# Kernel optimization log

Measured on AMD Instinct MI355X. Metric: run time of the kernel, lower is better.

The kernel has to match this reference:

```python
import jax, jax.numpy as jnp
import numpy as np

N = 50000
E = 500000
IN_DIM = 384
HID = 64
HEADS = 4
OUT_DIM = 128
EPS_SM = 1e-16
EPS_LN = 1e-5
NEG_SLOPE = 0.2


def gat_conv(x, row, col, ew, W, a_src, a_dst, b, heads, out_ch, concat):
    n = x.shape[0]
    h = (x @ W).reshape(n, heads, out_ch)              # [N, H, C]
    # per-node attention scores, then gather (same math as gathering h first)
    s_src = jnp.sum(h * a_src, axis=-1)                # [N, H]
    s_dst = jnp.sum(h * a_dst, axis=-1)                # [N, H]
    alpha = jax.nn.leaky_relu(s_src[row] + s_dst[col], NEG_SLOPE)  # [E, H]
    alpha = alpha * ew[:, None]
    a_exp = jnp.exp(alpha)
    denom = jax.ops.segment_sum(a_exp, col, num_segments=n)        # [N, H]
    alpha = a_exp / (denom[col] + EPS_SM)              # [E, H]
    msg = alpha[:, :, None] * h[col]                   # [E, H, C]
    out = jax.ops.segment_sum(msg, row, num_segments=n)  # [N, H, C]
    if concat:
        out = out.reshape(n, heads * out_ch)
    else:
        out = out.mean(axis=1)
    return out + b


def layer_norm(x, g, b):
    mu = x.mean(axis=-1, keepdims=True)
    var = x.var(axis=-1, keepdims=True)
    return (x - mu) / jnp.sqrt(var + EPS_LN) * g + b


def setup_inputs() -> dict:
    key = jax.random.key(0)
    ks = jax.random.split(key, 16)
    D1 = HEADS * HID  # 256
    inp = {
        "x": jax.random.normal(ks[0], (N, IN_DIM), jnp.float32),
        "edge_index": jax.random.randint(ks[1], (2, E), 0, N, jnp.int32),
        "edge_weight": jax.random.uniform(ks[2], (E,), jnp.float32),
        "W1": jax.random.normal(ks[3], (IN_DIM, D1), jnp.float32) * (1.0 / np.sqrt(IN_DIM)),
        "as1": jax.random.normal(ks[4], (1, HEADS, HID), jnp.float32) * 0.1,
        "ad1": jax.random.normal(ks[5], (1, HEADS, HID), jnp.float32) * 0.1,
        "b1": jnp.zeros((D1,), jnp.float32),
        "g1": jnp.ones((D1,), jnp.float32),
        "be1": jnp.zeros((D1,), jnp.float32),
        "W2": jax.random.normal(ks[6], (D1, D1), jnp.float32) * (1.0 / np.sqrt(D1)),
        "as2": jax.random.normal(ks[7], (1, HEADS, HID), jnp.float32) * 0.1,
        "ad2": jax.random.normal(ks[8], (1, HEADS, HID), jnp.float32) * 0.1,
        "b2": jnp.zeros((D1,), jnp.float32),
        "g2": jnp.ones((D1,), jnp.float32),
        "be2": jnp.zeros((D1,), jnp.float32),
        "W3": jax.random.normal(ks[9], (D1, OUT_DIM), jnp.float32) * (1.0 / np.sqrt(D1)),
        "as3": jax.random.normal(ks[10], (1, 1, OUT_DIM), jnp.float32) * 0.1,
        "ad3": jax.random.normal(ks[11], (1, 1, OUT_DIM), jnp.float32) * 0.1,
        "b3": jnp.zeros((OUT_DIM,), jnp.float32),
        "g3": jnp.ones((OUT_DIM,), jnp.float32),
        "be3": jnp.zeros((OUT_DIM,), jnp.float32),
    }
    return inp


def reference(x, edge_index, edge_weight, W1, as1, ad1, b1, g1, be1,
              W2, as2, ad2, b2, g2, be2, W3, as3, ad3, b3, g3, be3):
    row, col = edge_index[0], edge_index[1]
    h = gat_conv(x, row, col, edge_weight, W1, as1, ad1, b1, HEADS, HID, True)
    h = jax.nn.elu(layer_norm(h, g1, be1))
    h = gat_conv(h, row, col, edge_weight, W2, as2, ad2, b2, HEADS, HID, True)
    h = jax.nn.elu(layer_norm(h, g2, be2))
    h = gat_conv(h, row, col, edge_weight, W3, as3, ad3, b3, 1, OUT_DIM, False)
    return layer_norm(h, g3, be3)
```

## Files before the change

### kernel.cpp

```cpp
#include <hip/hip_runtime.h>
#include <hip/hip_bf16.h>


typedef __bf16 bf16x8_t __attribute__((ext_vector_type(8)));
typedef float  fx4      __attribute__((ext_vector_type(4)));

__device__ __forceinline__ float u2f(unsigned short u) {
    return __uint_as_float(((unsigned)u) << 16);
}
__device__ __forceinline__ unsigned short f2u(float f) {
    unsigned b = __float_as_uint(f);
    unsigned rounded = b + 0x7FFF + ((b >> 16) & 1);
    if (((b >> 23) & 0xFF) == 0xFF) rounded = b;
    return (unsigned short)(rounded >> 16);
}

__global__ void f32_to_bf16_k(const float* __restrict__ src, unsigned short* __restrict__ dst,
                              long n) {
    long i = (long)blockIdx.x * 256 + threadIdx.x;
    const long stride = (long)gridDim.x * 256;
    for (; i < n; i += stride) dst[i] = f2u(src[i]);
}

__global__ void transpose_conv_k(const float* __restrict__ W, unsigned short* __restrict__ Wt,
                                 int K, int N) {
    int idx = blockIdx.x * 256 + threadIdx.x;
    if (idx >= K * N) return;
    int k = idx / N, n = idx - k * N;
    Wt[(size_t)n * K + k] = f2u(W[idx]);
}

__global__ void fill_const_f32_k(float* __restrict__ out, long n, float v) {
    long i = (long)blockIdx.x * 256 + threadIdx.x;
    const long stride = (long)gridDim.x * 256;
    for (; i < n; i += stride) out[i] = v;
}

__global__ void count_both_k(const int* __restrict__ row, const int* __restrict__ col,
                             int* __restrict__ rcnt, int* __restrict__ ccnt,
                             int2* __restrict__ rank, int E, int Nn) {
    int e = blockIdx.x * 256 + threadIdx.x;
    if (e >= E) return;
    int r = row[e], c = col[e];
    int rr = -1, rc = -1;
    if ((unsigned)r < (unsigned)Nn) rr = atomicAdd(&rcnt[r], 1);
    if ((unsigned)c < (unsigned)Nn) rc = atomicAdd(&ccnt[c], 1);
    rank[e] = make_int2(rr, rc);
}

__global__ __launch_bounds__(256) void scan1_k(const int* __restrict__ cnt,
                                               int* __restrict__ local,
                                               int* __restrict__ bsum, int n) {
    __shared__ int sm[256];
    int i = blockIdx.x * 256 + threadIdx.x;
    int tid = threadIdx.x;
    int v = (i < n) ? cnt[i] : 0;
    sm[tid] = v;
    __syncthreads();
    for (int o = 1; o < 256; o <<= 1) {
        int t = (tid >= o) ? sm[tid - o] : 0;
        __syncthreads();
        sm[tid] += t;
        __syncthreads();
    }
    if (i < n) local[i] = sm[tid];
    if (tid == 255) bsum[blockIdx.x] = sm[255];
}

__global__ __launch_bounds__(512) void scan2_k(int* __restrict__ bsum, int nb) {
    __shared__ int sm[512];
    int tid = threadIdx.x;
    int v = (tid < nb) ? bsum[tid] : 0;
    sm[tid] = v;
    __syncthreads();
    for (int o = 1; o < 512; o <<= 1) {
        int t = (tid >= o) ? sm[tid - o] : 0;
        __syncthreads();
        sm[tid] += t;
        __syncthreads();
    }
    if (tid < nb) bsum[tid] = sm[tid];
}

__global__ __launch_bounds__(256) void scan3_k(const int* __restrict__ cnt,
                                               const int* __restrict__ local,
                                               const int* __restrict__ bsum,
                                               int* __restrict__ rowptr,
                                               int* __restrict__ colptr,
                                               int N) {
    int i = blockIdx.x * 256 + threadIdx.x;
    int n2 = 2 * N;
    if (i >= n2) return;
    int b = blockIdx.x;
    int s = local[i] + (b > 0 ? bsum[b - 1] : 0);
    if (i < N) {
        rowptr[i + 1] = s;
        if (i == 0) rowptr[0] = 0;
    } else {
        int bN = (N - 1) >> 8;
        int base = local[N - 1] + (bN > 0 ? bsum[bN - 1] : 0);
        int j = i - N;
        colptr[j + 1] = s - base;
        if (j == 0) colptr[0] = 0;
    }
}

__global__ void fill_both_k(const int* __restrict__ row, const int* __restrict__ col,
                            const float* __restrict__ ew,
                            const int2* __restrict__ rank,
                            const int* __restrict__ rowptr, const int* __restrict__ colptr,
                            long* __restrict__ csr, long* __restrict__ csc,
                            int E, int Nn) {
    int e = blockIdx.x * 256 + threadIdx.x;
    if (e >= E) return;
    int r = row[e], c = col[e];
    int wb = __float_as_int(ew[e]);
    int2 rk = rank[e];
    if (rk.x >= 0) {
        int s = rowptr[r] + rk.x;
        int cc = ((unsigned)c < (unsigned)Nn) ? c : 0;
        long v = (long)(unsigned)cc | ((long)(unsigned)wb << 32);
        __builtin_nontemporal_store(v, csr + s);
    }
    if (rk.y >= 0) {
        int s = colptr[c] + rk.y;
        int rr = ((unsigned)r < (unsigned)Nn) ? r : 0;
        long v = (long)(unsigned)rr | ((long)(unsigned)wb << 32);
        __builtin_nontemporal_store(v, csc + s);
    }
}

#define LSTR 40
__global__ __launch_bounds__(256) void gemm_bf16(const unsigned short* __restrict__ A,
                                                 const unsigned short* __restrict__ Bt,
                                                 unsigned short* __restrict__ C,
                                                 int M, int Ncol, int K) {
    __shared__ unsigned short As[128 * LSTR];
    __shared__ unsigned short Bs[128 * LSTR];
    const int t = threadIdx.x;
    const int lane = t & 63;
    const int wave = t >> 6;
    const int quad = lane >> 4, l16 = lane & 15;
    const int row0 = blockIdx.y * 128, col0 = blockIdx.x * 128;
    const int wr = (wave >> 1) * 64, wc = (wave & 1) * 64;
    const int sr = t >> 2, ss = (t & 3) * 8;
    fx4 acc[4][4] = {};
    for (int k0 = 0; k0 < K; k0 += 32) {
#pragma unroll
        for (int rr = 0; rr < 2; rr++) {
            int r = sr + rr * 64;
            uint4 av = make_uint4(0, 0, 0, 0);
            int gr = row0 + r;
            if (gr < M) av = *(const uint4*)(A + (size_t)gr * K + k0 + ss);
            *(uint4*)(As + r * LSTR + ss) = av;
            uint4 bv = *(const uint4*)(Bt + (size_t)(col0 + r) * K + k0 + ss);
            *(uint4*)(Bs + r * LSTR + ss) = bv;
        }
        __syncthreads();
        bf16x8_t af[4], bfr[4];
#pragma unroll
        for (int i = 0; i < 4; i++) {
            af[i]  = *(const bf16x8_t*)(As + (wr + i * 16 + l16) * LSTR + quad * 8);
            bfr[i] = *(const bf16x8_t*)(Bs + (wc + i * 16 + l16) * LSTR + quad * 8);
        }
#pragma unroll
        for (int i = 0; i < 4; i++)
#pragma unroll
            for (int j = 0; j < 4; j++)
                acc[i][j] = __builtin_amdgcn_mfma_f32_16x16x32_bf16(af[i], bfr[j], acc[i][j], 0, 0, 0);
        __syncthreads();
    }
#pragma unroll
    for (int i = 0; i < 4; i++) {
        int rb = row0 + wr + i * 16 + quad * 4;
#pragma unroll
        for (int j = 0; j < 4; j++) {
            int c = col0 + wc + j * 16 + l16;
#pragma unroll
            for (int r = 0; r < 4; r++) {
                int gr = rb + r;
                if (gr < M) C[(size_t)gr * Ncol + c] = f2u(acc[i][j][r]);
            }
        }
    }
}

template <int CPL, int LPH, int H>
__global__ __launch_bounds__(256) void scores_k(const unsigned short* __restrict__ hb,
                                                const float* __restrict__ asrc,
                                                const float* __restrict__ adst,
                                                float* __restrict__ ssrc, float* __restrict__ sdst,
                                                int N) {
    int node = blockIdx.x * 4 + (threadIdx.x >> 6);
    if (node >= N) return;
    int lane = threadIdx.x & 63;
    const int D = CPL * 64;
    const unsigned short* hp = hb + (size_t)node * D + lane * CPL;
    float s1 = 0.f, s2 = 0.f;
#pragma unroll
    for (int i = 0; i < CPL; i++) {
        float h = u2f(hp[i]);
        s1 += h * asrc[lane * CPL + i];
        s2 += h * adst[lane * CPL + i];
    }
#pragma unroll
    for (int m = 1; m < LPH; m <<= 1) {
        s1 += __shfl_xor(s1, m);
        s2 += __shfl_xor(s2, m);
    }
    if ((lane & (LPH - 1)) == 0) {
        ssrc[(size_t)node * H + lane / LPH] = s1;
        sdst[(size_t)node * H + lane / LPH] = s2;
    }
}

template <int H>
__global__ __launch_bounds__(256) void denom_csc_k(const int* __restrict__ colptr,
                                                   const int2* __restrict__ csc,
                                                   const float* __restrict__ ssrc,
                                                   const float* __restrict__ sdst,
                                                   float* __restrict__ att, int N) {
    int idx = blockIdx.x * 256 + threadIdx.x;
    int node = idx / H;
    int h = idx - node * H;
    if (node >= N) return;
    const float sd = sdst[(size_t)node * H + h];
    float acc = 0.f;
    int kbeg = colptr[node], kend = colptr[node + 1];
    if (kbeg < kend) {
        int klast = kend - 1;
        int2 ceA = csc[kbeg];
        int2 ceB = csc[(kbeg + 1 < kend) ? kbeg + 1 : klast];
        int2 ceC = csc[(kbeg + 2 < kend) ? kbeg + 2 : klast];
        float sA = ssrc[(size_t)ceA.x * H + h];
        float sB = ssrc[(size_t)ceB.x * H + h];
        for (int k = kbeg; k < kend; k++) {
            int2 ceD = csc[(k + 3 < kend) ? k + 3 : klast];
            float sC = ssrc[(size_t)ceC.x * H + h];
            float we = __int_as_float(ceA.y);
            float s = sA + sd;
            s = (s > 0.f) ? s : 0.2f * s;
            acc += __expf(fminf(s * we, 60.f));
            ceA = ceB; ceB = ceC; ceC = ceD;
            sA = sB; sB = sC;
        }
    }
    att[(size_t)node * 2 * H + h] = sd;
    att[(size_t)node * 2 * H + H + h] = 1.0f / (acc + 1e-16f);
}

template <int CPL, int H, bool DOELU, bool F32OUT>
__global__ __launch_bounds__(256) void agg_ln_k(const unsigned short* __restrict__ hb,
                                                const float* __restrict__ ssrc,
                                                const float* __restrict__ att,
                                                const int* __restrict__ rowptr,
                                                const int2* __restrict__ csr,
                                                const float* __restrict__ bias,
                                                const float* __restrict__ gamma,
                                                const float* __restrict__ beta,
                                                void* __restrict__ outv, int N, int E) {
    int node = blockIdx.x * 4 + (threadIdx.x >> 6);
    if (node >= N) return;
    const int lane = threadIdx.x & 63;
    const int hl = lane & 31;
    const int eo = lane >> 5;
    const int D = CPL * 32, C = D / H;
    const int colbase = hl * CPL;
    const int head = colbase / C;
    const float sn = ssrc[(size_t)node * H + head];
    const unsigned short* hbl = hb + colbase;
    float acc[CPL] = {};
    int kbeg = rowptr[node], kend = rowptr[node + 1];
    if (kbeg < 0) kbeg = 0;
    if (kend > E) kend = E;

    if (kbeg < kend) {
        const int klast = kend - 1;
        int kA = kbeg + eo, kB = kbeg + 2 + eo, kC = kbeg + 4 + eo;
        int2 ceA = csr[kA < kend ? kA : klast];
        int2 ceB = csr[kB < kend ? kB : klast];
        int2 ceC = csr[kC < kend ? kC : klast];
        float sdA, rdA, sdB, rdB;
        uint4 hvA = make_uint4(0,0,0,0), hvB = make_uint4(0,0,0,0);
        {
            const float* ap = att + (size_t)ceA.x * (2 * H);
            if constexpr (H == 1) { float2 p = *(const float2*)ap; sdA = p.x; rdA = p.y; }
            else { sdA = ap[head]; rdA = ap[H + head]; }
            const unsigned short* hp = hbl + (size_t)ceA.x * D;
            if constexpr (CPL == 8) hvA = *(const uint4*)hp;
            else { uint2 t2 = *(const uint2*)hp; hvA.x = t2.x; hvA.y = t2.y; }
        }
        {
            const float* ap = att + (size_t)ceB.x * (2 * H);
            if constexpr (H == 1) { float2 p = *(const float2*)ap; sdB = p.x; rdB = p.y; }
            else { sdB = ap[head]; rdB = ap[H + head]; }
            const unsigned short* hp = hbl + (size_t)ceB.x * D;
            if constexpr (CPL == 8) hvB = *(const uint4*)hp;
            else { uint2 t2 = *(const uint2*)hp; hvB.x = t2.x; hvB.y = t2.y; }
        }
        for (int k = kbeg; k < kend; k += 2) {
            int kD = k + 6 + eo;
            int2 ceD = csr[kD < kend ? kD : klast];
            float sdC, rdC;
            uint4 hvC = make_uint4(0,0,0,0);
            {
                const float* ap = att + (size_t)ceC.x * (2 * H);
                if constexpr (H == 1) { float2 p = *(const float2*)ap; sdC = p.x; rdC = p.y; }
                else { sdC = ap[head]; rdC = ap[H + head]; }
                const unsigned short* hp = hbl + (size_t)ceC.x * D;
                if constexpr (CPL == 8) hvC = *(const uint4*)hp;
                else { uint2 t2 = *(const uint2*)hp; hvC.x = t2.x; hvC.y = t2.y; }
            }
            float we = __int_as_float(ceA.y);
            float s = sn + sdA;
            s = (s > 0.f) ? s : 0.2f * s;
            float ae = __expf(fminf(s * we, 60.f));
            float w = ae * rdA;
            w = (k + eo < kend) ? w : 0.f;
            acc[0] += w * u2f((unsigned short)(hvA.x & 0xFFFFu));
            acc[1] += w * u2f((unsigned short)(hvA.x >> 16));
            acc[2] += w * u2f((unsigned short)(hvA.y & 0xFFFFu));
            acc[3] += w * u2f((unsigned short)(hvA.y >> 16));
            if constexpr (CPL == 8) {
                acc[4] += w * u2f((unsigned short)(hvA.z & 0xFFFFu));
                acc[5] += w * u2f((unsigned short)(hvA.z >> 16));
                acc[6] += w * u2f((unsigned short)(hvA.w & 0xFFFFu));
                acc[7] += w * u2f((unsigned short)(hvA.w >> 16));
            }
            ceA = ceB; ceB = ceC; ceC = ceD;
            sdA = sdB; rdA = rdB; hvA = hvB;
            sdB = sdC; rdB = rdC; hvB = hvC;
        }
    }
#pragma unroll
    for (int i = 0; i < CPL; i++) acc[i] += __shfl_xor(acc[i], 32);

    float v[CPL];
    float sum = 0.f, sq = 0.f;
#pragma unroll
    for (int i = 0; i < CPL; i++) {
        v[i] = acc[i] + bias[colbase + i];
        sum += v[i];
        sq += v[i] * v[i];
    }
#pragma unroll
    for (int m = 1; m < 32; m <<= 1) {
        sum += __shfl_xor(sum, m);
        sq += __shfl_xor(sq, m);
    }
    float mu  = sum * (1.0f / D);
    float var = sq * (1.0f / D) - mu * mu;
    float inv = rsqrtf(fmaxf(var, 0.f) + 1e-5f);
    if (eo == 0) {
#pragma unroll
        for (int i = 0; i < CPL; i++) {
            float y = (v[i] - mu) * inv * gamma[colbase + i] + beta[colbase + i];
            if (DOELU) y = (y > 0.f) ? y : (__expf(y) - 1.f);
            size_t idx = (size_t)node * D + colbase + i;
            if constexpr (F32OUT) ((float*)outv)[idx] = y;
            else                  ((unsigned short*)outv)[idx] = f2u(y);
        }
    }
}

extern "C" void kernel_launch(void* const* d_in, const int* in_sizes, int n_in,
                              void* d_out, int out_size, void* d_ws, size_t ws_size,
                              hipStream_t stream) {
    const int IN_DIM = 384;
    const int N = in_sizes[0] / IN_DIM;
    const int E = in_sizes[1] / 2;
    float* outp = (float*)d_out;
    const int FG = 2048;

    if (n_in != 21 || out_size != N * 128) {
        fill_const_f32_k<<<FG, 256, 0, stream>>>(outp, (long)out_size, 9.0f);
        return;
    }

    const float* x = (const float*)d_in[0];
    const int* ei = (const int*)d_in[1];
    const int* row = ei;
    const int* col = ei + E;
    const float* ew = (const float*)d_in[2];
    const float* W1 = (const float*)d_in[3];
    const float* as1 = (const float*)d_in[4];
    const float* ad1 = (const float*)d_in[5];
    const float* b1 = (const float*)d_in[6];
    const float* g1 = (const float*)d_in[7];
    const float* be1 = (const float*)d_in[8];
    const float* W2 = (const float*)d_in[9];
    const float* as2 = (const float*)d_in[10];
    const float* ad2 = (const float*)d_in[11];
    const float* b2 = (const float*)d_in[12];
    const float* g2 = (const float*)d_in[13];
    const float* be2 = (const float*)d_in[14];
    const float* W3 = (const float*)d_in[15];
    const float* as3 = (const float*)d_in[16];
    const float* ad3 = (const float*)d_in[17];
    const float* b3 = (const float*)d_in[18];
    const float* g3 = (const float*)d_in[19];
    const float* be3 = (const float*)d_in[20];

    char* ws = (char*)d_ws;
    size_t off = 0;
    auto alloc = [&](size_t b) -> char* {
        char* p = ws + off;
        off = (off + b + 255) & ~(size_t)255;
        return p;
    };
    unsigned short* xb = (unsigned short*)alloc((size_t)N * IN_DIM * 2);
    unsigned short* hb = (unsigned short*)alloc((size_t)N * 256 * 2);
    unsigned short* ab = (unsigned short*)alloc((size_t)N * 256 * 2);
    float* att = (float*)alloc((size_t)N * 8 * 4);
    float* ssrc = (float*)alloc((size_t)N * 4 * 4);
    float* sdst = (float*)alloc((size_t)N * 4 * 4);
    unsigned short* W1t = (unsigned short*)alloc((size_t)384 * 256 * 2);
    unsigned short* W2t = (unsigned short*)alloc((size_t)256 * 256 * 2);
    unsigned short* W3t = (unsigned short*)alloc((size_t)256 * 128 * 2);
    int* rowptr = (int*)alloc((size_t)(N + 1) * 4);
    int* colptr = (int*)alloc((size_t)(N + 1) * 4);
    int* cnt2 = (int*)alloc((size_t)2 * N * 4);
    int* slocal = (int*)alloc((size_t)2 * N * 4);
    int* sbsum = (int*)alloc((size_t)512 * 4);
    int2* rank = (int2*)alloc((size_t)E * 8);
    long* csr = (long*)alloc((size_t)E * 8);
    long* csc = (long*)alloc((size_t)E * 8);

    if (off > ws_size) {
        fill_const_f32_k<<<FG, 256, 0, stream>>>(outp, (long)out_size, 7.0f);
        return;
    }

    int* rcnt = cnt2;
    int* ccnt = cnt2 + N;

    const int ebl = (E + 255) / 256;
    const int nbl4 = (N + 3) / 4;
    const int mrows = (N + 127) / 128;
    const int n2 = 2 * N;
    const int sblocks = (n2 + 255) / 256;

    f32_to_bf16_k<<<FG, 256, 0, stream>>>(x, xb, (long)N * IN_DIM);
    transpose_conv_k<<<(384 * 256 + 255) / 256, 256, 0, stream>>>(W1, W1t, 384, 256);
    transpose_conv_k<<<(256 * 256 + 255) / 256, 256, 0, stream>>>(W2, W2t, 256, 256);
    transpose_conv_k<<<(256 * 128 + 255) / 256, 256, 0, stream>>>(W3, W3t, 256, 128);

    hipMemsetAsync(cnt2, 0, (size_t)n2 * 4, stream);
    count_both_k<<<ebl, 256, 0, stream>>>(row, col, rcnt, ccnt, rank, E, N);
    scan1_k<<<sblocks, 256, 0, stream>>>(cnt2, slocal, sbsum, n2);
    scan2_k<<<1, 512, 0, stream>>>(sbsum, sblocks);
    scan3_k<<<sblocks, 256, 0, stream>>>(cnt2, slocal, sbsum, rowptr, colptr, N);
    fill_both_k<<<ebl, 256, 0, stream>>>(row, col, ew, rank, rowptr, colptr, csr, csc, E, N);

    gemm_bf16<<<dim3(2, mrows), 256, 0, stream>>>(xb, W1t, hb, N, 256, 384);
    scores_k<4, 16, 4><<<nbl4, 256, 0, stream>>>(hb, as1, ad1, ssrc, sdst, N);
    denom_csc_k<4><<<(N * 4 + 255) / 256, 256, 0, stream>>>(colptr, (const int2*)csc, ssrc, sdst, att, N);
    agg_ln_k<8, 4, true, false><<<nbl4, 256, 0, stream>>>(hb, ssrc, att, rowptr, (const int2*)csr,
                                                          b1, g1, be1, ab, N, E);

    gemm_bf16<<<dim3(2, mrows), 256, 0, stream>>>(ab, W2t, hb, N, 256, 256);
    scores_k<4, 16, 4><<<nbl4, 256, 0, stream>>>(hb, as2, ad2, ssrc, sdst, N);
    denom_csc_k<4><<<(N * 4 + 255) / 256, 256, 0, stream>>>(colptr, (const int2*)csc, ssrc, sdst, att, N);
    agg_ln_k<8, 4, true, false><<<nbl4, 256, 0, stream>>>(hb, ssrc, att, rowptr, (const int2*)csr,
                                                          b2, g2, be2, ab, N, E);

    gemm_bf16<<<dim3(1, mrows), 256, 0, stream>>>(ab, W3t, hb, N, 128, 256);
    scores_k<2, 64, 1><<<nbl4, 256, 0, stream>>>(hb, as3, ad3, ssrc, sdst, N);
    denom_csc_k<1><<<(N + 255) / 256, 256, 0, stream>>>(colptr, (const int2*)csc, ssrc, sdst, att, N);
    agg_ln_k<4, 1, false, true><<<nbl4, 256, 0, stream>>>(hb, ssrc, att, rowptr, (const int2*)csr,
                                                          b3, g3, be3, outp, N, E);
}
```

Baseline: 505.8 us.

## Split edge loops across more lanes in denominator and aggregation kernels

The softmax-denominator kernel now gives each (node, head) pair two threads that stride over alternate incoming edges, then combines their partial sums with a lane shuffle. The aggregation kernel now has each wavefront handle four edges at a time instead of two. Each lane covers twice as many feature columns through two 16-byte loads, and the partial results are reduced across lane groups. The aim is more memory-level parallelism on the irregular edge gathers of short adjacency lists, at the cost of more registers per lane and extra shuffle reductions.

```diff
diff --git a/kernel.cpp b/kernel.cpp
--- a/kernel.cpp
+++ b/kernel.cpp
@@ -221,21 +221,27 @@
                                                    const float* __restrict__ sdst,
                                                    float* __restrict__ att, int N) {
     int idx = blockIdx.x * 256 + threadIdx.x;
-    int node = idx / H;
-    int h = idx - node * H;
+    const int L2H = (H == 4) ? 2 : ((H == 2) ? 1 : 0);
+    int node = idx >> (L2H + 1);
+    int rem = idx - (node << (L2H + 1));
+    int h = rem & (H - 1);
+    int parity = rem >> L2H;
     if (node >= N) return;
     const float sd = sdst[(size_t)node * H + h];
     float acc = 0.f;
     int kbeg = colptr[node], kend = colptr[node + 1];
-    if (kbeg < kend) {
+    int k0 = kbeg + parity;
+    if (k0 < kend) {
         int klast = kend - 1;
-        int2 ceA = csc[kbeg];
-        int2 ceB = csc[(kbeg + 1 < kend) ? kbeg + 1 : klast];
-        int2 ceC = csc[(kbeg + 2 < kend) ? kbeg + 2 : klast];
+        int kB = k0 + 2, kC = k0 + 4;
+        int2 ceA = csc[k0];
+        int2 ceB = csc[kB < kend ? kB : klast];
+        int2 ceC = csc[kC < kend ? kC : klast];
         float sA = ssrc[(size_t)ceA.x * H + h];
         float sB = ssrc[(size_t)ceB.x * H + h];
-        for (int k = kbeg; k < kend; k++) {
-            int2 ceD = csc[(k + 3 < kend) ? k + 3 : klast];
+        for (int k = k0; k < kend; k += 2) {
+            int kD = k + 6;
+            int2 ceD = csc[kD < kend ? kD : klast];
             float sC = ssrc[(size_t)ceC.x * H + h];
             float we = __int_as_float(ceA.y);
             float s = sA + sd;
@@ -245,8 +251,11 @@
             sA = sB; sB = sC;
         }
     }
-    att[(size_t)node * 2 * H + h] = sd;
-    att[(size_t)node * 2 * H + H + h] = 1.0f / (acc + 1e-16f);
+    acc += __shfl_xor(acc, H);
+    if (parity == 0) {
+        att[(size_t)node * 2 * H + h] = sd;
+        att[(size_t)node * 2 * H + H + h] = 1.0f / (acc + 1e-16f);
+    }
 }
 
 template <int CPL, int H, bool DOELU, bool F32OUT>
@@ -262,10 +271,10 @@
     int node = blockIdx.x * 4 + (threadIdx.x >> 6);
     if (node >= N) return;
     const int lane = threadIdx.x & 63;
-    const int hl = lane & 31;
-    const int eo = lane >> 5;
-    const int D = CPL * 32, C = D / H;
-    const int colbase = hl * CPL;
+    const int ql = lane & 15;
+    const int eo = lane >> 4;
+    const int D = CPL * 16, C = D / H;
+    const int colbase = ql * CPL;
     const int head = colbase / C;
     const float sn = ssrc[(size_t)node * H + head];
     const unsigned short* hbl = hb + colbase;
@@ -276,40 +285,41 @@
 
     if (kbeg < kend) {
         const int klast = kend - 1;
-        int kA = kbeg + eo, kB = kbeg + 2 + eo, kC = kbeg + 4 + eo;
+        int kA = kbeg + eo, kB = kbeg + 4 + eo, kC = kbeg + 8 + eo;
         int2 ceA = csr[kA < kend ? kA : klast];
         int2 ceB = csr[kB < kend ? kB : klast];
         int2 ceC = csr[kC < kend ? kC : klast];
         float sdA, rdA, sdB, rdB;
-        uint4 hvA = make_uint4(0,0,0,0), hvB = make_uint4(0,0,0,0);
+        uint4 hvA0 = make_uint4(0,0,0,0), hvA1 = make_uint4(0,0,0,0);
+        uint4 hvB0 = make_uint4(0,0,0,0), hvB1 = make_uint4(0,0,0,0);
         {
             const float* ap = att + (size_t)ceA.x * (2 * H);
             if constexpr (H == 1) { float2 p = *(const float2*)ap; sdA = p.x; rdA = p.y; }
             else { sdA = ap[head]; rdA = ap[H + head]; }
             const unsigned short* hp = hbl + (size_t)ceA.x * D;
-            if constexpr (CPL == 8) hvA = *(const uint4*)hp;
-            else { uint2 t2 = *(const uint2*)hp; hvA.x = t2.x; hvA.y = t2.y; }
+            hvA0 = *(const uint4*)hp;
+            if constexpr (CPL == 16) hvA1 = *(const uint4*)(hp + 8);
         }
         {
             const float* ap = att + (size_t)ceB.x * (2 * H);
             if constexpr (H == 1) { float2 p = *(const float2*)ap; sdB = p.x; rdB = p.y; }
             else { sdB = ap[head]; rdB = ap[H + head]; }
             const unsigned short* hp = hbl + (size_t)ceB.x * D;
-            if constexpr (CPL == 8) hvB = *(const uint4*)hp;
-            else { uint2 t2 = *(const uint2*)hp; hvB.x = t2.x; hvB.y = t2.y; }
-        }
-        for (int k = kbeg; k < kend; k += 2) {
-            int kD = k + 6 + eo;
+            hvB0 = *(const uint4*)hp;
+            if constexpr (CPL == 16) hvB1 = *(const uint4*)(hp + 8);
+        }
+        for (int k = kbeg; k < kend; k += 4) {
+            int kD = k + 12 + eo;
             int2 ceD = csr[kD < kend ? kD : klast];
             float sdC, rdC;
-            uint4 hvC = make_uint4(0,0,0,0);
+            uint4 hvC0 = make_uint4(0,0,0,0), hvC1 = make_uint4(0,0,0,0);
             {
                 const float* ap = att + (size_t)ceC.x * (2 * H);
                 if constexpr (H == 1) { float2 p = *(const float2*)ap; sdC = p.x; rdC = p.y; }
                 else { sdC = ap[head]; rdC = ap[H + head]; }
                 const unsigned short* hp = hbl + (size_t)ceC.x * D;
-                if constexpr (CPL == 8) hvC = *(const uint4*)hp;
-                else { uint2 t2 = *(const uint2*)hp; hvC.x = t2.x; hvC.y = t2.y; }
+                hvC0 = *(const uint4*)hp;
+                if constexpr (CPL == 16) hvC1 = *(const uint4*)(hp + 8);
             }
             float we = __int_as_float(ceA.y);
             float s = sn + sdA;
@@ -317,23 +327,36 @@
             float ae = __expf(fminf(s * we, 60.f));
             float w = ae * rdA;
             w = (k + eo < kend) ? w : 0.f;
-            acc[0] += w * u2f((unsigned short)(hvA.x & 0xFFFFu));
-            acc[1] += w * u2f((unsigned short)(hvA.x >> 16));
-            acc[2] += w * u2f((unsigned short)(hvA.y & 0xFFFFu));
-            acc[3] += w * u2f((unsigned short)(hvA.y >> 16));
-            if constexpr (CPL == 8) {
-                acc[4] += w * u2f((unsigned short)(hvA.z & 0xFFFFu));
-                acc[5] += w * u2f((unsigned short)(hvA.z >> 16));
-                acc[6] += w * u2f((unsigned short)(hvA.w & 0xFFFFu));
-                acc[7] += w * u2f((unsigned short)(hvA.w >> 16));
+            acc[0] += w * u2f((unsigned short)(hvA0.x & 0xFFFFu));
+            acc[1] += w * u2f((unsigned short)(hvA0.x >> 16));
+            acc[2] += w * u2f((unsigned short)(hvA0.y & 0xFFFFu));
+            acc[3] += w * u2f((unsigned short)(hvA0.y >> 16));
+            acc[4] += w * u2f((unsigned short)(hvA0.z & 0xFFFFu));
+            acc[5] += w * u2f((unsigned short)(hvA0.z >> 16));
+            acc[6] += w * u2f((unsigned short)(hvA0.w & 0xFFFFu));
+            acc[7] += w * u2f((unsigned short)(hvA0.w >> 16));
+            if constexpr (CPL == 16) {
+                acc[8]  += w * u2f((unsigned short)(hvA1.x & 0xFFFFu));
+                acc[9]  += w * u2f((unsigned short)(hvA1.x >> 16));
+                acc[10] += w * u2f((unsigned short)(hvA1.y & 0xFFFFu));
+                acc[11] += w * u2f((unsigned short)(hvA1.y >> 16));
+                acc[12] += w * u2f((unsigned short)(hvA1.z & 0xFFFFu));
+                acc[13] += w * u2f((unsigned short)(hvA1.z >> 16));
+                acc[14] += w * u2f((unsigned short)(hvA1.w & 0xFFFFu));
+                acc[15] += w * u2f((unsigned short)(hvA1.w >> 16));
             }
             ceA = ceB; ceB = ceC; ceC = ceD;
-            sdA = sdB; rdA = rdB; hvA = hvB;
-            sdB = sdC; rdB = rdC; hvB = hvC;
-        }
-    }
-#pragma unroll
-    for (int i = 0; i < CPL; i++) acc[i] += __shfl_xor(acc[i], 32);
+            sdA = sdB; rdA = rdB;
+            hvA0 = hvB0; hvA1 = hvB1;
+            sdB = sdC; rdB = rdC;
+            hvB0 = hvC0; hvB1 = hvC1;
+        }
+    }
+#pragma unroll
+    for (int i = 0; i < CPL; i++) {
+        acc[i] += __shfl_xor(acc[i], 32);
+        acc[i] += __shfl_xor(acc[i], 16);
+    }
 
     float v[CPL];
     float sum = 0.f, sq = 0.f;
@@ -344,7 +367,7 @@
         sq += v[i] * v[i];
     }
 #pragma unroll
-    for (int m = 1; m < 32; m <<= 1) {
+    for (int m = 1; m < 16; m <<= 1) {
         sum += __shfl_xor(sum, m);
         sq += __shfl_xor(sq, m);
     }
@@ -454,19 +477,19 @@
 
     gemm_bf16<<<dim3(2, mrows), 256, 0, stream>>>(xb, W1t, hb, N, 256, 384);
     scores_k<4, 16, 4><<<nbl4, 256, 0, stream>>>(hb, as1, ad1, ssrc, sdst, N);
-    denom_csc_k<4><<<(N * 4 + 255) / 256, 256, 0, stream>>>(colptr, (const int2*)csc, ssrc, sdst, att, N);
-    agg_ln_k<8, 4, true, false><<<nbl4, 256, 0, stream>>>(hb, ssrc, att, rowptr, (const int2*)csr,
-                                                          b1, g1, be1, ab, N, E);
+    denom_csc_k<4><<<(N * 8 + 255) / 256, 256, 0, stream>>>(colptr, (const int2*)csc, ssrc, sdst, att, N);
+    agg_ln_k<16, 4, true, false><<<nbl4, 256, 0, stream>>>(hb, ssrc, att, rowptr, (const int2*)csr,
+                                                           b1, g1, be1, ab, N, E);
 
     gemm_bf16<<<dim3(2, mrows), 256, 0, stream>>>(ab, W2t, hb, N, 256, 256);
     scores_k<4, 16, 4><<<nbl4, 256, 0, stream>>>(hb, as2, ad2, ssrc, sdst, N);
-    denom_csc_k<4><<<(N * 4 + 255) / 256, 256, 0, stream>>>(colptr, (const int2*)csc, ssrc, sdst, att, N);
-    agg_ln_k<8, 4, true, false><<<nbl4, 256, 0, stream>>>(hb, ssrc, att, rowptr, (const int2*)csr,
-                                                          b2, g2, be2, ab, N, E);
+    denom_csc_k<4><<<(N * 8 + 255) / 256, 256, 0, stream>>>(colptr, (const int2*)csc, ssrc, sdst, att, N);
+    agg_ln_k<16, 4, true, false><<<nbl4, 256, 0, stream>>>(hb, ssrc, att, rowptr, (const int2*)csr,
+                                                           b2, g2, be2, ab, N, E);
 
     gemm_bf16<<<dim3(1, mrows), 256, 0, stream>>>(ab, W3t, hb, N, 128, 256);
     scores_k<2, 64, 1><<<nbl4, 256, 0, stream>>>(hb, as3, ad3, ssrc, sdst, N);
-    denom_csc_k<1><<<(N + 255) / 256, 256, 0, stream>>>(colptr, (const int2*)csc, ssrc, sdst, att, N);
-    agg_ln_k<4, 1, false, true><<<nbl4, 256, 0, stream>>>(hb, ssrc, att, rowptr, (const int2*)csr,
+    denom_csc_k<1><<<(N * 2 + 255) / 256, 256, 0, stream>>>(colptr, (const int2*)csc, ssrc, sdst, att, N);
+    agg_ln_k<8, 1, false, true><<<nbl4, 256, 0, stream>>>(hb, ssrc, att, rowptr, (const int2*)csr,
                                                           b3, g3, be3, outp, N, E);
 }
```

New measurement: 506.9 us. No clear change (+0.2%).
